# Kernel optimization log

Measured on AMD Instinct MI355X. Metric: run time of the kernel, lower is better.

Reference implementation:

```python
import jax, jax.numpy as jnp
import numpy as np

MAX_DISP = 40   # corr(40,1,40,1,1): max horizontal displacement (stereo disparity)
SLOPE = 0.1     # LeakyReLU negative slope


def _compress(x, W, b):
    # 3x3 conv, stride 1, pad 1 (NCHW), then LeakyReLU(0.1)
    y = jax.lax.conv_general_dilated(
        x, W, window_strides=(1, 1), padding=((1, 1), (1, 1)),
        dimension_numbers=('NCHW', 'OIHW', 'NCHW'))
    y = y + b[None, :, None, None]
    return jnp.where(y >= 0, y, SLOPE * y)


def _corr1d(a, b):
    # 1-D horizontal correlation (DispNetC style): for disparity d in [0, MAX_DISP],
    # corr[:, d, y, x] = mean_c a[:, c, y, x] * b[:, c, y, x - d], zero-padded.
    B, C, H, Wd = a.shape
    bp = jnp.pad(b, ((0, 0), (0, 0), (0, 0), (MAX_DISP, 0)))
    outs = [
        jnp.mean(a * jax.lax.dynamic_slice_in_dim(bp, MAX_DISP - d, Wd, axis=3), axis=1)
        for d in range(MAX_DISP + 1)
    ]  # small fixed loop over 41 displacements
    return jnp.stack(outs, axis=1)  # [B, 41, H, W]


def setup_inputs() -> dict:
    key = jax.random.key(0)
    k1, k2, k3 = jax.random.split(key, 3)
    B, C, H, W = 8, 64, 192, 384
    conv1a = jax.random.normal(k1, (B, C, H, W), dtype=jnp.float32)
    conv1b = jax.random.normal(k2, (B, C, H, W), dtype=jnp.float32)
    W_comp = jax.random.normal(k3, (16, 64, 3, 3), dtype=jnp.float32) * 0.05
    b_comp = jnp.zeros((16,), dtype=jnp.float32)
    return {"conv1a": conv1a, "conv1b": conv1b, "W_comp": W_comp, "b_comp": b_comp}


def reference(conv1a, conv1b, W_comp, b_comp):
    a_mini = _compress(conv1a, W_comp, b_comp)  # [B,16,H,W]
    b_mini = _compress(conv1b, W_comp, b_comp)  # shared weights, as in the module
    return _corr1d(a_mini, b_mini)              # [B,41,H,W]
```

## Files before the change

### kernel.cpp

```cpp
#include <hip/hip_runtime.h>
#include <hip/hip_bf16.h>

#define B_   8
#define CIN  64
#define CM   16
#define H_   192
#define W_   384
#define ND   41
#define HW   (H_ * W_)
#define SLOPE 0.1f
#define SMINI ((size_t)B_ * CM * H_ * W_)

typedef __attribute__((ext_vector_type(8))) short short8v;
typedef __attribute__((ext_vector_type(4))) float floatx4;

__device__ __forceinline__ float bf2f(short h) {
    union { unsigned u; float f; } cv;
    cv.u = ((unsigned)(unsigned short)h) << 16;
    return cv.f;
}
__device__ __forceinline__ short f2bf(float f) {
    __hip_bfloat16 h = __float2bfloat16(f);
    return *(short*)&h;
}

__global__ void wprep_kernel(const float* __restrict__ w, short* __restrict__ wbf) {
    int i = blockIdx.x * 256 + threadIdx.x;
    if (i >= CM * 576) return;
    int co = i / 576, k = i - co * 576;
    int t = k >> 6, c = k & 63;
    wbf[i] = f2bf(w[(co * CIN + c) * 9 + t]);
}

#define YT 6
#define XT 32
#define LC 34
#define PSTR 72

__global__ __launch_bounds__(256, 4) void conv_mfma(
    const float* __restrict__ ina, const float* __restrict__ inb,
    const short* __restrict__ wbf, const float* __restrict__ bias,
    short* __restrict__ mini)
{
    __shared__ __align__(16) short px[8 * LC * PSTR];

    int blk = blockIdx.x;
    int xt = blk % 12;  blk /= 12;
    int yt = blk % 32;  blk /= 32;
    int b  = blk & 7;
    int t  = blk >> 3;
    const float* src = t ? inb : ina;
    int x0 = xt * XT, y0 = yt * YT;
    int tid = threadIdx.x;

    #pragma unroll
    for (int i = 0; i < 17; ++i) {
        int e = i * 256 + tid;
        int lx = e % LC;
        int rcq = e / LC;
        int row = rcq >> 4;
        int c0 = (rcq & 15) << 2;
        int gy = y0 - 1 + row;
        int gx = x0 - 1 + lx;
        float v0 = 0.f, v1 = 0.f, v2 = 0.f, v3 = 0.f;
        if ((unsigned)gy < (unsigned)H_ && (unsigned)gx < (unsigned)W_) {
            const float* p = src + ((size_t)(b * CIN + c0)) * HW + (size_t)gy * W_ + gx;
            v0 = p[0]; v1 = p[HW]; v2 = p[2 * HW]; v3 = p[3 * HW];
        }
        short4 q;
        q.x = f2bf(v0); q.y = f2bf(v1); q.z = f2bf(v2); q.w = f2bf(v3);
        *(short4*)(px + (row * LC + lx) * PSTR + c0) = q;
    }

    int lane = tid & 63;
    int n16  = lane & 15;
    int quad = lane >> 4;

    short8v af[18];
    #pragma unroll
    for (int ks = 0; ks < 18; ++ks)
        af[ks] = *(const short8v*)(wbf + n16 * 576 + ks * 32 + quad * 8);

    __syncthreads();

    int wv = tid >> 6;
    floatx4 acc[3] = {{0,0,0,0},{0,0,0,0},{0,0,0,0}};
    int base[3];
    #pragma unroll
    for (int j = 0; j < 3; ++j) {
        int mt = wv * 3 + j;
        int r = mt >> 1, xb = (mt & 1) << 4;
        base[j] = (r * LC + xb + n16) * PSTR + quad * 8;
    }
    #pragma unroll
    for (int ks = 0; ks < 18; ++ks) {
        const int tap = ks >> 1, ch = ks & 1;
        const int dy = tap / 3, dx = tap % 3;
        const int off = (dy * LC + dx) * PSTR + ch * 32;
        #pragma unroll
        for (int j = 0; j < 3; ++j) {
            short8v bfr = *(const short8v*)(px + base[j] + off);
            acc[j] = __builtin_amdgcn_mfma_f32_16x16x32_bf16(af[ks], bfr, acc[j], 0, 0, 0);
        }
    }

    float bia[4];
    #pragma unroll
    for (int i = 0; i < 4; ++i) bia[i] = bias[quad * 4 + i];
    #pragma unroll
    for (int j = 0; j < 3; ++j) {
        int mt = wv * 3 + j;
        int r = mt >> 1, xb = (mt & 1) << 4;
        int y = y0 + r, x = x0 + xb + n16;
        size_t o = (((size_t)(t * B_ + b) * H_ + y) * W_ + x) * CM + quad * 4;
        short4 q;
        float v;
        v = acc[j][0] + bia[0]; v = v >= 0.f ? v : SLOPE * v; q.x = f2bf(v);
        v = acc[j][1] + bia[1]; v = v >= 0.f ? v : SLOPE * v; q.y = f2bf(v);
        v = acc[j][2] + bia[2]; v = v >= 0.f ? v : SLOPE * v; q.z = f2bf(v);
        v = acc[j][3] + bia[3]; v = v >= 0.f ? v : SLOPE * v; q.w = f2bf(v);
        *(short4*)(mini + o) = q;
    }
}

#define BSTR 24

__global__ __launch_bounds__(384) void corr_nhwc(
    const short* __restrict__ mini, float* __restrict__ out)
{
    __shared__ __align__(16) short bl[W_ * BSTR];
    int b = blockIdx.x / H_;
    int y = blockIdx.x % H_;
    int x = threadIdx.x;

    size_t arow = ((size_t)b * H_ + y) * W_ * CM;
    size_t brow = ((size_t)(B_ + b) * H_ + y) * W_ * CM;

    short8v p0 = *(const short8v*)(mini + brow + (size_t)x * CM);
    short8v p1 = *(const short8v*)(mini + brow + (size_t)x * CM + 8);
    *(short8v*)(bl + x * BSTR) = p0;
    *(short8v*)(bl + x * BSTR + 8) = p1;

    float av[16];
    short8v a0 = *(const short8v*)(mini + arow + (size_t)x * CM);
    short8v a1 = *(const short8v*)(mini + arow + (size_t)x * CM + 8);
    #pragma unroll
    for (int i = 0; i < 8; ++i) { av[i] = bf2f(a0[i]); av[8 + i] = bf2f(a1[i]); }

    __syncthreads();

    float* ob = out + ((size_t)b * ND * H_ + y) * W_ + x;
    #pragma unroll 1
    for (int d = 0; d < ND; ++d) {
        float s = 0.f;
        int xs = x - d;
        if (xs >= 0) {
            const short* bp = bl + xs * BSTR;
            short8v c0 = *(const short8v*)bp;
            short8v c1 = *(const short8v*)(bp + 8);
            float s0 = 0.f, s1 = 0.f;
            #pragma unroll
            for (int i = 0; i < 8; ++i) {
                s0 += av[i]     * bf2f(c0[i]);
                s1 += av[8 + i] * bf2f(c1[i]);
            }
            s = s0 + s1;
        }
        ob[(size_t)d * HW] = s * 0.0625f;
    }
}

extern "C" void kernel_launch(void* const* d_in, const int* in_sizes, int n_in,
                              void* d_out, int out_size, void* d_ws, size_t ws_size,
                              hipStream_t stream) {
    const float* conv1a = (const float*)d_in[0];
    const float* conv1b = (const float*)d_in[1];
    const float* W_comp = (const float*)d_in[2];
    const float* b_comp = (const float*)d_in[3];
    float* out = (float*)d_out;

    short* mini = (short*)d_ws;
    short* wbf  = mini + 2 * SMINI;

    wprep_kernel<<<36, 256, 0, stream>>>(W_comp, wbf);
    conv_mfma<<<2 * B_ * 32 * 12, 256, 0, stream>>>(conv1a, conv1b, wbf, b_comp, mini);
    corr_nhwc<<<B_ * H_, 384, 0, stream>>>(mini, out);
}
```

Before: 437.9 us.

## Load conv inputs directly from global, swizzle blocks, use fp32 LDS in correlation

The conv kernel no longer stages a bf16 input tile in shared memory. Each MFMA B-fragment is now loaded straight from global memory and converted in registers, and the weights are pre-swizzled so that each lane loads its A-fragment with a single vector read. Block indices are remapped so that neighbouring blocks land on different XCDs/partitions, and the correlation kernel stores the b row as fp32 in LDS so the inner loop uses float4 reads without conversion. The aim is to remove LDS staging, syncthreads and convert overhead, at the cost of many redundant, strided global loads (9 taps reread the same pixels) that rely on cache hits.

```diff
diff --git a/kernel.cpp b/kernel.cpp
--- a/kernel.cpp
+++ b/kernel.cpp
@@ -24,83 +24,70 @@
     return *(short*)&h;
 }
 
-__global__ void wprep_kernel(const float* __restrict__ w, short* __restrict__ wbf) {
+__global__ void wprep_kernel(const float* __restrict__ w, short* __restrict__ wbf2) {
     int i = blockIdx.x * 256 + threadIdx.x;
-    if (i >= CM * 576) return;
-    int co = i / 576, k = i - co * 576;
-    int t = k >> 6, c = k & 63;
-    wbf[i] = f2bf(w[(co * CIN + c) * 9 + t]);
+    if (i >= 18 * 512) return;
+    int ks = i >> 9;
+    int r  = i & 511;
+    int n16  = r >> 5;
+    int quad = (r >> 3) & 3;
+    int u    = r & 7;
+    int c   = (ks & 1) * 32 + quad * 8 + u;
+    int tap = ks >> 1;
+    int o = ks * 512 + (quad * 16 + n16) * 8 + u;
+    wbf2[o] = f2bf(w[(n16 * CIN + c) * 9 + tap]);
 }
 
-#define YT 6
-#define XT 32
-#define LC 34
-#define PSTR 72
-
-__global__ __launch_bounds__(256, 4) void conv_mfma(
+__global__ __launch_bounds__(256, 4) void conv_direct(
     const float* __restrict__ ina, const float* __restrict__ inb,
-    const short* __restrict__ wbf, const float* __restrict__ bias,
+    const short* __restrict__ wbf2, const float* __restrict__ bias,
     short* __restrict__ mini)
 {
-    __shared__ __align__(16) short px[8 * LC * PSTR];
-
-    int blk = blockIdx.x;
+    int blk = (blockIdx.x & 7) * 768 + (blockIdx.x >> 3);
     int xt = blk % 12;  blk /= 12;
     int yt = blk % 32;  blk /= 32;
     int b  = blk & 7;
     int t  = blk >> 3;
     const float* src = t ? inb : ina;
-    int x0 = xt * XT, y0 = yt * YT;
+    int x0 = xt * 32, y0 = yt * 6;
     int tid = threadIdx.x;
+    int lane = tid & 63, wv = tid >> 6;
+    int n16 = lane & 15, quad = lane >> 4;
 
-    #pragma unroll
-    for (int i = 0; i < 17; ++i) {
-        int e = i * 256 + tid;
-        int lx = e % LC;
-        int rcq = e / LC;
-        int row = rcq >> 4;
-        int c0 = (rcq & 15) << 2;
-        int gy = y0 - 1 + row;
-        int gx = x0 - 1 + lx;
-        float v0 = 0.f, v1 = 0.f, v2 = 0.f, v3 = 0.f;
-        if ((unsigned)gy < (unsigned)H_ && (unsigned)gx < (unsigned)W_) {
-            const float* p = src + ((size_t)(b * CIN + c0)) * HW + (size_t)gy * W_ + gx;
-            v0 = p[0]; v1 = p[HW]; v2 = p[2 * HW]; v3 = p[3 * HW];
-        }
-        short4 q;
-        q.x = f2bf(v0); q.y = f2bf(v1); q.z = f2bf(v2); q.w = f2bf(v3);
-        *(short4*)(px + (row * LC + lx) * PSTR + c0) = q;
-    }
+    const float* sb = src + (size_t)b * CIN * HW;
 
-    int lane = tid & 63;
-    int n16  = lane & 15;
-    int quad = lane >> 4;
-
-    short8v af[18];
-    #pragma unroll
-    for (int ks = 0; ks < 18; ++ks)
-        af[ks] = *(const short8v*)(wbf + n16 * 576 + ks * 32 + quad * 8);
-
-    __syncthreads();
-
-    int wv = tid >> 6;
     floatx4 acc[3] = {{0,0,0,0},{0,0,0,0},{0,0,0,0}};
-    int base[3];
+    int rs[3], xs[3];
     #pragma unroll
     for (int j = 0; j < 3; ++j) {
         int mt = wv * 3 + j;
-        int r = mt >> 1, xb = (mt & 1) << 4;
-        base[j] = (r * LC + xb + n16) * PSTR + quad * 8;
+        rs[j] = mt >> 1;
+        xs[j] = x0 + ((mt & 1) << 4) + n16;
     }
+
     #pragma unroll
     for (int ks = 0; ks < 18; ++ks) {
-        const int tap = ks >> 1, ch = ks & 1;
+        const int tap = ks >> 1, h = ks & 1;
         const int dy = tap / 3, dx = tap % 3;
-        const int off = (dy * LC + dx) * PSTR + ch * 32;
+        const int cbase = h * 32 + quad * 8;
+        short8v af = *(const short8v*)(wbf2 + ks * 512 + lane * 8);
+        const float* cb = sb + (size_t)cbase * HW;
         #pragma unroll
         for (int j = 0; j < 3; ++j) {
-            short8v bfr = *(const short8v*)(px + base[j] + off);
-            acc[j] = __builtin_amdgcn_mfma_f32_16x16x32_bf16(af[ks], bfr, acc[j], 0, 0, 0);
+            int yy = y0 + rs[j] + dy - 1;
+            if ((unsigned)yy < (unsigned)H_) {
+                int xx = xs[j] + dx - 1;
+                bool ok = (unsigned)xx < (unsigned)W_;
+                int xxc = ok ? xx : 0;
+                const float* p = cb + (size_t)yy * W_ + xxc;
+                float v[8];
+                #pragma unroll
+                for (int u = 0; u < 8; ++u) v[u] = p[(size_t)u * HW];
+                short8v bfr;
+                #pragma unroll
+                for (int u = 0; u < 8; ++u) bfr[u] = f2bf(ok ? v[u] : 0.f);
+                acc[j] = __builtin_amdgcn_mfma_f32_16x16x32_bf16(af, bfr, acc[j], 0, 0, 0);
+            }
         }
     }
 
@@ -123,23 +110,23 @@
     }
 }
 
-#define BSTR 24
-
-__global__ __launch_bounds__(384) void corr_nhwc(
+#define CST 20
+__global__ __launch_bounds__(384) void corr_f32(
     const short* __restrict__ mini, float* __restrict__ out)
 {
-    __shared__ __align__(16) short bl[W_ * BSTR];
+    __shared__ __align__(16) float bl[W_ * CST];
     int b = blockIdx.x / H_;
     int y = blockIdx.x % H_;
     int x = threadIdx.x;
 
-    size_t arow = ((size_t)b * H_ + y) * W_ * CM;
-    size_t brow = ((size_t)(B_ + b) * H_ + y) * W_ * CM;
+    size_t arow = ((size_t)b * H_ + y) * (size_t)W_ * CM;
+    size_t brow = ((size_t)(B_ + b) * H_ + y) * (size_t)W_ * CM;
 
     short8v p0 = *(const short8v*)(mini + brow + (size_t)x * CM);
     short8v p1 = *(const short8v*)(mini + brow + (size_t)x * CM + 8);
-    *(short8v*)(bl + x * BSTR) = p0;
-    *(short8v*)(bl + x * BSTR + 8) = p1;
+    float* bw = bl + x * CST;
+    #pragma unroll
+    for (int i = 0; i < 8; ++i) { bw[i] = bf2f(p0[i]); bw[8 + i] = bf2f(p1[i]); }
 
     float av[16];
     short8v a0 = *(const short8v*)(mini + arow + (size_t)x * CM);
@@ -155,16 +142,12 @@
         float s = 0.f;
         int xs = x - d;
         if (xs >= 0) {
-            const short* bp = bl + xs * BSTR;
-            short8v c0 = *(const short8v*)bp;
-            short8v c1 = *(const short8v*)(bp + 8);
-            float s0 = 0.f, s1 = 0.f;
-            #pragma unroll
-            for (int i = 0; i < 8; ++i) {
-                s0 += av[i]     * bf2f(c0[i]);
-                s1 += av[8 + i] * bf2f(c1[i]);
-            }
-            s = s0 + s1;
+            const float4* bp = (const float4*)(bl + xs * CST);
+            float4 b0 = bp[0], b1 = bp[1], b2 = bp[2], b3 = bp[3];
+            s  = av[0]  * b0.x + av[1]  * b0.y + av[2]  * b0.z + av[3]  * b0.w;
+            s += av[4]  * b1.x + av[5]  * b1.y + av[6]  * b1.z + av[7]  * b1.w;
+            s += av[8]  * b2.x + av[9]  * b2.y + av[10] * b2.z + av[11] * b2.w;
+            s += av[12] * b3.x + av[13] * b3.y + av[14] * b3.z + av[15] * b3.w;
         }
         ob[(size_t)d * HW] = s * 0.0625f;
     }
@@ -180,9 +163,9 @@
     float* out = (float*)d_out;
 
     short* mini = (short*)d_ws;
-    short* wbf  = mini + 2 * SMINI;
+    short* wbf2 = mini + 2 * SMINI;
 
-    wprep_kernel<<<36, 256, 0, stream>>>(W_comp, wbf);
-    conv_mfma<<<2 * B_ * 32 * 12, 256, 0, stream>>>(conv1a, conv1b, wbf, b_comp, mini);
-    corr_nhwc<<<B_ * H_, 384, 0, stream>>>(mini, out);
+    wprep_kernel<<<36, 256, 0, stream>>>(W_comp, wbf2);
+    conv_direct<<<2 * B_ * 32 * 12, 256, 0, stream>>>(conv1a, conv1b, wbf2, b_comp, mini);
+    corr_f32<<<B_ * H_, 384, 0, stream>>>(mini, out);
 }
```

Result: slower. 712.5 us (+62.7%).
